# Performance work log

Hardware: AMD Instinct MI355X
Metric: run time of the kernel (lower is better)

The kernel has to match this reference:

```python
import jax, jax.numpy as jnp
import numpy as np

N, K, DIN, DOUT = 50000, 16, 128, 64  # nodes per graph, fixed in-degree, feature dims


def setup_inputs() -> dict:
    key = jax.random.key(0)
    ks = jax.random.split(key, 9)
    s1 = 1.0 / np.sqrt(DIN)
    s2 = 1.0 / np.sqrt(2 * DOUT)
    return {
        "x1": jax.random.normal(ks[0], (N, DIN), jnp.float32),
        "x2": jax.random.normal(ks[1], (N, DIN), jnp.float32),
        "nbr1": jax.random.randint(ks[2], (N, K), 0, N, dtype=jnp.int32),
        "nbr2": jax.random.randint(ks[3], (N, K), 0, N, dtype=jnp.int32),
        "W_e1": jax.random.uniform(ks[4], (DIN, DOUT), jnp.float32, -s1, s1),
        "W_s1": jax.random.uniform(ks[5], (DIN, DOUT), jnp.float32, -s1, s1),
        "W_e2": jax.random.uniform(ks[6], (2 * DOUT, DOUT), jnp.float32, -s2, s2),
        "W_s2": jax.random.uniform(ks[7], (2 * DOUT, DOUT), jnp.float32, -s2, s2),
        "w_att": jax.random.uniform(ks[8], (2 * DOUT,), jnp.float32, -s2, s2),
    }


def _layer(x, nbr, We, Ws, norm):
    # CGNNConv: per-edge-type linear on sources, self linear on dests,
    # norm-weighted scatter-add aggregation, sigmoid(cat(self, aggr)).
    xn = x @ We                                      # [N, DOUT] source transform
    xs = x @ Ws                                      # [N, DOUT] self transform
    aggr = jnp.sum(norm[..., None] * xn[nbr], axis=1)  # [N, DOUT] fixed-degree segment sum
    return jax.nn.sigmoid(jnp.concatenate([xs, aggr], axis=1)), aggr


def _self_attn(aggr, nbr, w):
    # exp(leaky_relu(cat(aggr[dst], aggr[src]) @ w)), normalized over each dst's in-edges
    si = aggr @ w[:DOUT]            # dest contribution, [N]
    sj = (aggr @ w[DOUT:])[nbr]     # src contribution,  [N, K]
    e = jnp.exp(jax.nn.leaky_relu(si[:, None] + sj, 0.01))
    return e / jnp.sum(e, axis=1, keepdims=True)


def _cross_attn(aggr1, nbr1, aggr2, nbr2):
    # pairwise exp(-||a1_k - a2_l||) over each paired node's neighbor sets,
    # normalized by the total sum; att1 = row marginals, att2 = col marginals.
    a1, a2 = aggr1[nbr1], aggr2[nbr2]                # [N, K, DOUT]
    d2 = (jnp.sum(a1 * a1, -1)[:, :, None] + jnp.sum(a2 * a2, -1)[:, None, :]
          - 2.0 * jnp.einsum('nkd,nld->nkl', a1, a2))
    sim = jnp.exp(-jnp.sqrt(jnp.maximum(d2, 1e-12)))  # [N, K, K]
    total = jnp.sum(sim, axis=(1, 2), keepdims=True)  # [N, 1, 1]
    att1 = jnp.sum(sim, axis=2) / total[:, :, 0]      # [N, K]
    att2 = jnp.sum(sim, axis=1) / total[:, 0, :]      # [N, K]
    return att1, att2


def reference(x1, x2, nbr1, nbr2, W_e1, W_s1, W_e2, W_s2, w_att):
    inv_deg = jnp.full((N, K), 1.0 / K, dtype=x1.dtype)  # degree(col)^-1 with fixed degree K
    # layers 0 .. num_layers-2 use degree norm (shared weights across both graphs)
    h1, aggr1 = _layer(x1, nbr1, W_e1, W_s1, inv_deg)
    h2, aggr2 = _layer(x2, nbr2, W_e1, W_s1, inv_deg)
    # attention stages on last aggregates
    sa1 = _self_attn(aggr1, nbr1, w_att)
    sa2 = _self_attn(aggr2, nbr2, w_att)
    ca1, ca2 = _cross_attn(aggr1, nbr1, aggr2, nbr2)
    # final layer uses norm = cross_attention * self_attention per edge
    o1, _ = _layer(h1, nbr1, W_e2, W_s2, ca1 * sa1)
    o2, _ = _layer(h2, nbr2, W_e2, W_s2, ca2 * sa2)
    return o1, o2
```

## Files before the change

kernel.cpp:

```cpp
#include <hip/hip_runtime.h>
#include <hip/hip_bf16.h>

#define N_NODES 50000
#define K_NBR   16
#define DIN     128
#define DOUT    64
#define NPB     64

typedef __hip_bfloat16 bf16;
typedef __attribute__((ext_vector_type(8))) short bf16x8;
typedef __attribute__((ext_vector_type(4))) float f32x4;

__device__ __forceinline__ float b2f(bf16 v) { return __bfloat162float(v); }
__device__ __forceinline__ float sigmoidf_(float x) { return 1.0f / (1.0f + __expf(-x)); }
__device__ __forceinline__ short f2bs(float f) {
    bf16 b = __float2bfloat16(f);
    return *reinterpret_cast<short*>(&b);
}

template <typename T> __device__ __forceinline__ float ld(const T* p, size_t i);
template <> __device__ __forceinline__ float ld<float>(const float* p, size_t i) { return p[i]; }
template <> __device__ __forceinline__ float ld<bf16>(const bf16* p, size_t i)   { return b2f(p[i]); }

template <typename T> __device__ __forceinline__ void st(T* p, size_t i, float v);
template <> __device__ __forceinline__ void st<float>(float* p, size_t i, float v) { p[i] = v; }
template <> __device__ __forceinline__ void st<bf16>(bf16* p, size_t i, float v)   { p[i] = __float2bfloat16(v); }

__device__ __forceinline__ bf16x8 load_a8(const bf16* p) { return *(const bf16x8*)p; }
__device__ __forceinline__ bf16x8 load_a8(const float* p) {
    float4 v0 = *(const float4*)p;
    float4 v1 = *(const float4*)(p + 4);
    bf16x8 r;
    r[0] = f2bs(v0.x); r[1] = f2bs(v0.y); r[2] = f2bs(v0.z); r[3] = f2bs(v0.w);
    r[4] = f2bs(v1.x); r[5] = f2bs(v1.y); r[6] = f2bs(v1.z); r[7] = f2bs(v1.w);
    return r;
}

__global__ __launch_bounds__(256) void wtrans_kernel(
    const void* __restrict__ Wa, const void* __restrict__ Wb,
    const void* __restrict__ Wc, const void* __restrict__ Wd,
    const unsigned short* __restrict__ x1probe,
    unsigned short* __restrict__ wtg, int* __restrict__ flag)
{
    __shared__ unsigned short t[DIN][DOUT + 1];
    __shared__ int cnt;
    if (threadIdx.x == 0) cnt = 0;
    __syncthreads();
    int c = 0;
#pragma unroll
    for (int i = 0; i < 16; ++i) {
        unsigned short w = x1probe[(size_t)(threadIdx.x * 16 + i) * 2];
        int e = (w >> 7) & 0xFF;
        c += (e >= 112 && e <= 142) ? 1 : 0;
    }
    atomicAdd(&cnt, c);
    __syncthreads();
    const int isf32 = (cnt >= 2048) ? 0 : 1;
    if (blockIdx.x == 0 && threadIdx.x == 0) *flag = isf32;

    const void* W = (blockIdx.x == 0 ? Wa : blockIdx.x == 1 ? Wb : blockIdx.x == 2 ? Wc : Wd);
    unsigned short* o = wtg + (size_t)blockIdx.x * DIN * DOUT;
    if (isf32) {
        const float* Wf = (const float*)W;
#pragma unroll 8
        for (int it = 0; it < 32; ++it) {
            int idx = threadIdx.x + 256 * it;
            t[idx >> 6][idx & 63] = (unsigned short)f2bs(Wf[idx]);
        }
    } else {
        const unsigned short* Wh = (const unsigned short*)W;
#pragma unroll 8
        for (int it = 0; it < 32; ++it) {
            int idx = threadIdx.x + 256 * it;
            t[idx >> 6][idx & 63] = Wh[idx];
        }
    }
    __syncthreads();
#pragma unroll 8
    for (int it = 0; it < 32; ++it) {
        int idx = threadIdx.x + 256 * it;
        int d = idx >> 7, k = idx & 127;
        o[idx] = t[k][d];
    }
}

template <typename TX, typename TO>
__device__ __forceinline__ void lin_mfma_body(
    const TX* __restrict__ x,
    const unsigned short* __restrict__ wt2,
    bf16* __restrict__ xnh, TO* __restrict__ o,
    unsigned short* __restrict__ wt)
{
    const int tid = threadIdx.x;
    const int nbase = blockIdx.x * NPB;

#pragma unroll
    for (int it = 0; it < 8; ++it) {
        int idx = tid + 256 * it;
        int mt = idx >> 10, rem = idx & 1023;
        int r = rem >> 4, c = rem & 15;
        int4 v = *(const int4*)(wt2 + mt * 8192 + r * DIN + c * 8);
        *(int4*)(wt + mt * 8192 + r * DIN + ((c ^ (r & 15)) << 3)) = v;
    }
    __syncthreads();

    const int w = tid >> 6, lane = tid & 63;
    const int m = lane & 15, g = lane >> 4;

    int arow = nbase + w * 16 + m;
    if (arow >= N_NODES) arow = N_NODES - 1;
    const TX* xrow = x + (size_t)arow * DIN;

    f32x4 acc[2][4] = {};
#pragma unroll
    for (int ks = 0; ks < 4; ++ks) {
        bf16x8 a = load_a8(xrow + ks * 32 + g * 8);
        int slot = ((ks * 4 + g) ^ m) << 3;
#pragma unroll
        for (int mt = 0; mt < 2; ++mt)
#pragma unroll
        for (int nc = 0; nc < 4; ++nc) {
            bf16x8 b = *(const bf16x8*)(wt + mt * 8192 + (nc * 16 + m) * DIN + slot);
            acc[mt][nc] = __builtin_amdgcn_mfma_f32_16x16x32_bf16(a, b, acc[mt][nc], 0, 0, 0);
        }
    }

#pragma unroll
    for (int nc = 0; nc < 4; ++nc) {
#pragma unroll
        for (int j = 0; j < 4; ++j) {
            int n = nbase + w * 16 + g * 4 + j;
            if (n < N_NODES) {
                int d = nc * 16 + m;
                xnh[(size_t)n * DOUT + d] = __float2bfloat16(acc[0][nc][j]);
                st(o, (size_t)n * DIN + d, sigmoidf_(acc[1][nc][j]));
            }
        }
    }
}

__global__ __launch_bounds__(256) void lin1_kernel(
    const void* __restrict__ x1, const void* __restrict__ x2,
    const unsigned short* __restrict__ wtg,
    bf16* __restrict__ xnh1, bf16* __restrict__ xnh2,
    bf16* __restrict__ h1, bf16* __restrict__ h2,
    const int* __restrict__ flag)
{
    __shared__ __align__(16) unsigned short wt[2 * DOUT * DIN];
    const int g = blockIdx.y;
    const void* x   = g ? x2 : x1;
    bf16*       xnh = g ? xnh2 : xnh1;
    bf16*       h   = g ? h2 : h1;
    if (*flag) lin_mfma_body<float, bf16>((const float*)x, wtg, xnh, h, wt);
    else       lin_mfma_body<bf16,  bf16>((const bf16*)x,  wtg, xnh, h, wt);
}

__global__ __launch_bounds__(256) void lin2_kernel(
    const bf16* __restrict__ h1, const bf16* __restrict__ h2,
    const unsigned short* __restrict__ wtg,
    bf16* __restrict__ heh1, bf16* __restrict__ heh2,
    void* __restrict__ out, const int* __restrict__ flag)
{
    __shared__ __align__(16) unsigned short wt[2 * DOUT * DIN];
    const int g = blockIdx.y;
    const bf16* h   = g ? h2 : h1;
    bf16*       heh = g ? heh2 : heh1;
    if (*flag) lin_mfma_body<bf16, float>(h, wtg + 2 * 8192, heh,
                                          (float*)out + (size_t)g * N_NODES * DIN, wt);
    else       lin_mfma_body<bf16, bf16>(h, wtg + 2 * 8192, heh,
                                         (bf16*)out + (size_t)g * N_NODES * DIN, wt);
}

template <typename T>
__device__ __forceinline__ void aggr1_body(
    const int* __restrict__ nbr, const bf16* __restrict__ xnh,
    bf16* __restrict__ agh, bf16* __restrict__ h, const T* __restrict__ watt,
    float* __restrict__ qq, float* __restrict__ slo, float* __restrict__ shi)
{
    const int warp = __builtin_amdgcn_readfirstlane(threadIdx.x >> 6);
    const int lane = threadIdx.x & 63;
    const int n = blockIdx.x * 4 + warp;
    const int* __restrict__ nrow = nbr + n * K_NBR;

    float acc = 0.f;
#pragma unroll
    for (int k = 0; k < K_NBR; ++k) {
        int idx = nrow[k];
        acc += b2f(xnh[(size_t)idx * DOUT + lane]);
    }
    acc *= (1.0f / K_NBR);
    bf16 av16 = __float2bfloat16(acc);
    float av = b2f(av16);
    agh[(size_t)n * DOUT + lane] = av16;
    h[(size_t)n * DIN + DOUT + lane] = __float2bfloat16(sigmoidf_(acc));

    float wl = ld(watt, lane);
    float wh = ld(watt, DOUT + lane);
    float pq = av * av;
    float pl = acc * wl;
    float ph = acc * wh;
#pragma unroll
    for (int off = 1; off < 64; off <<= 1) {
        pq += __shfl_xor(pq, off, 64);
        pl += __shfl_xor(pl, off, 64);
        ph += __shfl_xor(ph, off, 64);
    }
    if (lane == 0) { qq[n] = pq; slo[n] = pl; shi[n] = ph; }
}

__global__ __launch_bounds__(256) void aggr1_kernel(
    const int* __restrict__ nbr1, const int* __restrict__ nbr2,
    const bf16* __restrict__ xnh1, const bf16* __restrict__ xnh2,
    bf16* __restrict__ agh1, bf16* __restrict__ agh2,
    bf16* __restrict__ h1, bf16* __restrict__ h2,
    const void* __restrict__ watt,
    float* __restrict__ qq1, float* __restrict__ qq2,
    float* __restrict__ slo1, float* __restrict__ slo2,
    float* __restrict__ shi1, float* __restrict__ shi2,
    const int* __restrict__ flag)
{
    const int g = blockIdx.y;
    const int*  nbr = g ? nbr2 : nbr1;
    const bf16* xnh = g ? xnh2 : xnh1;
    bf16*       agh = g ? agh2 : agh1;
    bf16*       h   = g ? h2 : h1;
    float* qq  = g ? qq2  : qq1;
    float* slo = g ? slo2 : slo1;
    float* shi = g ? shi2 : shi1;
    if (*flag) aggr1_body<float>(nbr, xnh, agh, h, (const float*)watt, qq, slo, shi);
    else       aggr1_body<bf16>(nbr, xnh, agh, h, (const bf16*)watt,  qq, slo, shi);
}

__global__ __launch_bounds__(256) void attn_kernel(
    const int* __restrict__ nbr1, const int* __restrict__ nbr2,
    const unsigned short* __restrict__ agh1, const unsigned short* __restrict__ agh2,
    const float* __restrict__ qq1, const float* __restrict__ qq2,
    const float* __restrict__ slo1, const float* __restrict__ slo2,
    const float* __restrict__ shi1, const float* __restrict__ shi2,
    float* __restrict__ norm1, float* __restrict__ norm2)
{
    const int warp = threadIdx.x >> 6;
    const int lane = threadIdx.x & 63;
    const int n = blockIdx.x * 4 + warp;
    const int m = lane & 15, g = lane >> 4;

    int idxr = 0;
    if (lane < 32) idxr = ((lane < 16) ? nbr1 : nbr2)[n * K_NBR + m];

    const int i1 = __shfl(idxr, m, 64);
    const int i2 = __shfl(idxr, 16 + m, 64);

    const bf16x8* a1p = (const bf16x8*)(agh1 + (size_t)i1 * DOUT + g * 8);
    const bf16x8* a2p = (const bf16x8*)(agh2 + (size_t)i2 * DOUT + g * 8);
    bf16x8 aA = a1p[0], aB = a1p[4];
    bf16x8 bA = a2p[0], bB = a2p[4];

    int myidx = __shfl(idxr, lane & 31, 64);
    const float* pa = (lane < 16) ? qq1 : (lane < 32) ? qq2 : (lane < 48) ? shi1 : shi2;
    float aux = pa[(size_t)myidx];

    float si  = (lane < 16) ? slo1[n] : slo2[n];
    float sjv = __shfl(aux, 32 + (lane & 31), 64);
    float v = si + sjv;
    v = v > 0.f ? v : 0.01f * v;
    float ev = __expf(v);
    float esum = ev;
#pragma unroll
    for (int off = 1; off < 16; off <<= 1) esum += __shfl_xor(esum, off, 64);

    f32x4 acc = {};
    acc = __builtin_amdgcn_mfma_f32_16x16x32_bf16(aA, bA, acc, 0, 0, 0);
    acc = __builtin_amdgcn_mfma_f32_16x16x32_bf16(aB, bB, acc, 0, 0, 0);

    float q2c = __shfl(aux, 16 + m, 64);
    float s0, s1, s2, s3;
    {
        float q10 = __shfl(aux, g * 4 + 0, 64);
        float q11 = __shfl(aux, g * 4 + 1, 64);
        float q12 = __shfl(aux, g * 4 + 2, 64);
        float q13 = __shfl(aux, g * 4 + 3, 64);
        s0 = __expf(-sqrtf(fmaxf(q10 + q2c - 2.f * acc[0], 1e-12f)));
        s1 = __expf(-sqrtf(fmaxf(q11 + q2c - 2.f * acc[1], 1e-12f)));
        s2 = __expf(-sqrtf(fmaxf(q12 + q2c - 2.f * acc[2], 1e-12f)));
        s3 = __expf(-sqrtf(fmaxf(q13 + q2c - 2.f * acc[3], 1e-12f)));
    }

    float c = s0 + s1 + s2 + s3;
#pragma unroll
    for (int off = 1; off < 16; off <<= 1) {
        s0 += __shfl_xor(s0, off, 64);
        s1 += __shfl_xor(s1, off, 64);
        s2 += __shfl_xor(s2, off, 64);
        s3 += __shfl_xor(s3, off, 64);
    }
    float cs = c;
    cs += __shfl_xor(cs, 16, 64);
    cs += __shfl_xor(cs, 32, 64);
    float tot = cs;
#pragma unroll
    for (int off = 1; off < 16; off <<= 1) tot += __shfl_xor(tot, off, 64);
    float rt = 1.0f / tot;

    if (g == 1) norm2[(size_t)n * K_NBR + m] = cs * rt * ev / esum;

    float r0 = __shfl(s0, (m >> 2) << 4, 64);
    float r1 = __shfl(s1, (m >> 2) << 4, 64);
    float r2 = __shfl(s2, (m >> 2) << 4, 64);
    float r3 = __shfl(s3, (m >> 2) << 4, 64);
    int mr = m & 3;
    float rsm = mr == 0 ? r0 : mr == 1 ? r1 : mr == 2 ? r2 : r3;
    if (g == 0) norm1[(size_t)n * K_NBR + m] = rsm * rt * ev / esum;
}

template <typename T>
__device__ __forceinline__ void aggr2_body(
    const int* __restrict__ nbr, const bf16* __restrict__ heh,
    const float* __restrict__ nm, T* __restrict__ o)
{
    const int warp = __builtin_amdgcn_readfirstlane(threadIdx.x >> 6);
    const int lane = threadIdx.x & 63;
    const int n = blockIdx.x * 4 + warp;
    const int*   __restrict__ nrow = nbr + n * K_NBR;
    const float* __restrict__ wrow = nm + n * K_NBR;

    float acc = 0.f;
#pragma unroll
    for (int k = 0; k < K_NBR; ++k) {
        int   idx = nrow[k];
        float w   = wrow[k];
        acc += w * b2f(heh[(size_t)idx * DOUT + lane]);
    }
    st(o, (size_t)n * DIN + DOUT + lane, sigmoidf_(acc));
}

__global__ __launch_bounds__(256) void aggr2_kernel(
    const int* __restrict__ nbr1, const int* __restrict__ nbr2,
    const bf16* __restrict__ heh1, const bf16* __restrict__ heh2,
    const float* __restrict__ nm1, const float* __restrict__ nm2,
    void* __restrict__ out, const int* __restrict__ flag)
{
    const int g = blockIdx.y;
    const int*  nbr = g ? nbr2 : nbr1;
    const bf16* heh = g ? heh2 : heh1;
    const float* nm = g ? nm2 : nm1;
    if (*flag) aggr2_body<float>(nbr, heh, nm, (float*)out + (size_t)g * N_NODES * DIN);
    else       aggr2_body<bf16>(nbr, heh, nm, (bf16*)out + (size_t)g * N_NODES * DIN);
}

extern "C" void kernel_launch(void* const* d_in, const int* in_sizes, int n_in,
                              void* d_out, int out_size, void* d_ws, size_t ws_size,
                              hipStream_t stream)
{
    const void* x1   = d_in[0];
    const void* x2   = d_in[1];
    const int*  nbr1 = (const int*)d_in[2];
    const int*  nbr2 = (const int*)d_in[3];
    const void* We1  = d_in[4];
    const void* Ws1  = d_in[5];
    const void* We2  = d_in[6];
    const void* Ws2  = d_in[7];
    const void* watt = d_in[8];

    char* ws = (char*)d_ws;
    const size_t SZH  = (size_t)N_NODES * DOUT * sizeof(bf16);
    const size_t HSZ  = (size_t)N_NODES * DIN * sizeof(bf16);
    const size_t NMSZ = (size_t)N_NODES * K_NBR * sizeof(float);
    const size_t NSZ  = (size_t)N_NODES * sizeof(float);
    bf16* xnh1 = (bf16*)(ws + 0 * SZH);
    bf16* xnh2 = (bf16*)(ws + 1 * SZH);
    bf16* agh1 = (bf16*)(ws + 2 * SZH);
    bf16* agh2 = (bf16*)(ws + 3 * SZH);
    bf16* h1   = (bf16*)(ws + 4 * SZH);
    bf16* h2   = (bf16*)(ws + 4 * SZH + HSZ);
    char* p    =         ws + 4 * SZH + 2 * HSZ;
    float* nm1 = (float*)(p);
    float* nm2 = (float*)(p + NMSZ);
    int*  flag = (int*)  (p + 2 * NMSZ);
    char* aux  =          p + 2 * NMSZ + 4096;
    float* qq1  = (float*)(aux + 0 * NSZ);
    float* qq2  = (float*)(aux + 1 * NSZ);
    float* slo1 = (float*)(aux + 2 * NSZ);
    float* slo2 = (float*)(aux + 3 * NSZ);
    float* shi1 = (float*)(aux + 4 * NSZ);
    float* shi2 = (float*)(aux + 5 * NSZ);
    unsigned short* wtg = (unsigned short*)(aux + 6 * NSZ);

    dim3 b(256);
    dim3 g4(N_NODES / 4, 2);
    dim3 gl((N_NODES + NPB - 1) / NPB, 2);
    dim3 ga(N_NODES / 4);

    wtrans_kernel<<<dim3(4), b, 0, stream>>>(We1, Ws1, We2, Ws2,
                                             (const unsigned short*)x1, wtg, flag);
    lin1_kernel <<<gl, b, 0, stream>>>(x1, x2, wtg, xnh1, xnh2, h1, h2, flag);
    aggr1_kernel<<<g4, b, 0, stream>>>(nbr1, nbr2, xnh1, xnh2, agh1, agh2, h1, h2,
                                       watt, qq1, qq2, slo1, slo2, shi1, shi2, flag);
    attn_kernel <<<ga, b, 0, stream>>>(nbr1, nbr2, (const unsigned short*)agh1,
                                       (const unsigned short*)agh2, qq1, qq2,
                                       slo1, slo2, shi1, shi2, nm1, nm2);
    lin2_kernel <<<gl, b, 0, stream>>>(h1, h2, wtg, xnh1, xnh2, d_out, flag);
    aggr2_kernel<<<g4, b, 0, stream>>>(nbr1, nbr2, xnh1, xnh2, nm1, nm2, d_out, flag);
}
```

Baseline: 238.5 us.

## Fuse attention normalization into final-layer aggregation kernel

After: 230.6 us. 3.3% less time.

```diff
diff --git a/kernel.cpp b/kernel.cpp
--- a/kernel.cpp
+++ b/kernel.cpp
@@ -16,6 +16,9 @@
 __device__ __forceinline__ short f2bs(float f) {
     bf16 b = __float2bfloat16(f);
     return *reinterpret_cast<short*>(&b);
+}
+__device__ __forceinline__ float readlane_f(float v, int lane) {
+    return __uint_as_float(__builtin_amdgcn_readlane(__float_as_uint(v), lane));
 }
 
 template <typename T> __device__ __forceinline__ float ld(const T* p, size_t i);
@@ -231,15 +234,17 @@
     else       aggr1_body<bf16>(nbr, xnh, agh, h, (const bf16*)watt,  qq, slo, shi);
 }
 
-__global__ __launch_bounds__(256) void attn_kernel(
+template <typename TO>
+__device__ __forceinline__ void attn_fused_body(
     const int* __restrict__ nbr1, const int* __restrict__ nbr2,
     const unsigned short* __restrict__ agh1, const unsigned short* __restrict__ agh2,
     const float* __restrict__ qq1, const float* __restrict__ qq2,
     const float* __restrict__ slo1, const float* __restrict__ slo2,
     const float* __restrict__ shi1, const float* __restrict__ shi2,
-    float* __restrict__ norm1, float* __restrict__ norm2)
-{
-    const int warp = threadIdx.x >> 6;
+    const bf16* __restrict__ heh1, const bf16* __restrict__ heh2,
+    TO* __restrict__ out)
+{
+    const int warp = __builtin_amdgcn_readfirstlane(threadIdx.x >> 6);
     const int lane = threadIdx.x & 63;
     const int n = blockIdx.x * 4 + warp;
     const int m = lane & 15, g = lane >> 4;
@@ -301,50 +306,45 @@
     for (int off = 1; off < 16; off <<= 1) tot += __shfl_xor(tot, off, 64);
     float rt = 1.0f / tot;
 
-    if (g == 1) norm2[(size_t)n * K_NBR + m] = cs * rt * ev / esum;
-
     float r0 = __shfl(s0, (m >> 2) << 4, 64);
     float r1 = __shfl(s1, (m >> 2) << 4, 64);
     float r2 = __shfl(s2, (m >> 2) << 4, 64);
     float r3 = __shfl(s3, (m >> 2) << 4, 64);
     int mr = m & 3;
     float rsm = mr == 0 ? r0 : mr == 1 ? r1 : mr == 2 ? r2 : r3;
-    if (g == 0) norm1[(size_t)n * K_NBR + m] = rsm * rt * ev / esum;
-}
-
-template <typename T>
-__device__ __forceinline__ void aggr2_body(
-    const int* __restrict__ nbr, const bf16* __restrict__ heh,
-    const float* __restrict__ nm, T* __restrict__ o)
-{
-    const int warp = __builtin_amdgcn_readfirstlane(threadIdx.x >> 6);
-    const int lane = threadIdx.x & 63;
-    const int n = blockIdx.x * 4 + warp;
-    const int*   __restrict__ nrow = nbr + n * K_NBR;
-    const float* __restrict__ wrow = nm + n * K_NBR;
-
-    float acc = 0.f;
+
+    float wv = (g == 0) ? (rsm * rt * ev / esum)
+             : (g == 1) ? (cs  * rt * ev / esum) : 0.f;
+
+    const int* __restrict__ nrow1 = nbr1 + n * K_NBR;
+    const int* __restrict__ nrow2 = nbr2 + n * K_NBR;
+    float acc1 = 0.f, acc2 = 0.f;
 #pragma unroll
     for (int k = 0; k < K_NBR; ++k) {
-        int   idx = nrow[k];
-        float w   = wrow[k];
-        acc += w * b2f(heh[(size_t)idx * DOUT + lane]);
-    }
-    st(o, (size_t)n * DIN + DOUT + lane, sigmoidf_(acc));
-}
-
-__global__ __launch_bounds__(256) void aggr2_kernel(
+        float w1k = readlane_f(wv, k);
+        float w2k = readlane_f(wv, 16 + k);
+        int j1 = nrow1[k];
+        int j2 = nrow2[k];
+        acc1 += w1k * b2f(heh1[(size_t)j1 * DOUT + lane]);
+        acc2 += w2k * b2f(heh2[(size_t)j2 * DOUT + lane]);
+    }
+    st(out, (size_t)n * DIN + DOUT + lane, sigmoidf_(acc1));
+    st(out, ((size_t)N_NODES + n) * DIN + DOUT + lane, sigmoidf_(acc2));
+}
+
+__global__ __launch_bounds__(256) void attn_kernel(
     const int* __restrict__ nbr1, const int* __restrict__ nbr2,
+    const unsigned short* __restrict__ agh1, const unsigned short* __restrict__ agh2,
+    const float* __restrict__ qq1, const float* __restrict__ qq2,
+    const float* __restrict__ slo1, const float* __restrict__ slo2,
+    const float* __restrict__ shi1, const float* __restrict__ shi2,
     const bf16* __restrict__ heh1, const bf16* __restrict__ heh2,
-    const float* __restrict__ nm1, const float* __restrict__ nm2,
     void* __restrict__ out, const int* __restrict__ flag)
 {
-    const int g = blockIdx.y;
-    const int*  nbr = g ? nbr2 : nbr1;
-    const bf16* heh = g ? heh2 : heh1;
-    const float* nm = g ? nm2 : nm1;
-    if (*flag) aggr2_body<float>(nbr, heh, nm, (float*)out + (size_t)g * N_NODES * DIN);
-    else       aggr2_body<bf16>(nbr, heh, nm, (bf16*)out + (size_t)g * N_NODES * DIN);
+    if (*flag) attn_fused_body<float>(nbr1, nbr2, agh1, agh2, qq1, qq2, slo1, slo2,
+                                      shi1, shi2, heh1, heh2, (float*)out);
+    else       attn_fused_body<bf16>(nbr1, nbr2, agh1, agh2, qq1, qq2, slo1, slo2,
+                                     shi1, shi2, heh1, heh2, (bf16*)out);
 }
 
 extern "C" void kernel_launch(void* const* d_in, const int* in_sizes, int n_in,
@@ -364,7 +364,6 @@
     char* ws = (char*)d_ws;
     const size_t SZH  = (size_t)N_NODES * DOUT * sizeof(bf16);
     const size_t HSZ  = (size_t)N_NODES * DIN * sizeof(bf16);
-    const size_t NMSZ = (size_t)N_NODES * K_NBR * sizeof(float);
     const size_t NSZ  = (size_t)N_NODES * sizeof(float);
     bf16* xnh1 = (bf16*)(ws + 0 * SZH);
     bf16* xnh2 = (bf16*)(ws + 1 * SZH);
@@ -373,10 +372,8 @@
     bf16* h1   = (bf16*)(ws + 4 * SZH);
     bf16* h2   = (bf16*)(ws + 4 * SZH + HSZ);
     char* p    =         ws + 4 * SZH + 2 * HSZ;
-    float* nm1 = (float*)(p);
-    float* nm2 = (float*)(p + NMSZ);
-    int*  flag = (int*)  (p + 2 * NMSZ);
-    char* aux  =          p + 2 * NMSZ + 4096;
+    int*  flag = (int*)  (p);
+    char* aux  =          p + 4096;
     float* qq1  = (float*)(aux + 0 * NSZ);
     float* qq2  = (float*)(aux + 1 * NSZ);
     float* slo1 = (float*)(aux + 2 * NSZ);
@@ -395,9 +392,9 @@
     lin1_kernel <<<gl, b, 0, stream>>>(x1, x2, wtg, xnh1, xnh2, h1, h2, flag);
     aggr1_kernel<<<g4, b, 0, stream>>>(nbr1, nbr2, xnh1, xnh2, agh1, agh2, h1, h2,
                                        watt, qq1, qq2, slo1, slo2, shi1, shi2, flag);
+    lin2_kernel <<<gl, b, 0, stream>>>(h1, h2, wtg, xnh1, xnh2, d_out, flag);
     attn_kernel <<<ga, b, 0, stream>>>(nbr1, nbr2, (const unsigned short*)agh1,
                                        (const unsigned short*)agh2, qq1, qq2,
-                                       slo1, slo2, shi1, shi2, nm1, nm2);
-    lin2_kernel <<<gl, b, 0, stream>>>(h1, h2, wtg, xnh1, xnh2, d_out, flag);
-    aggr2_kernel<<<g4, b, 0, stream>>>(nbr1, nbr2, xnh1, xnh2, nm1, nm2, d_out, flag);
-}
+                                       slo1, slo2, shi1, shi2, xnh1, xnh2,
+                                       d_out, flag);
+}
```
